# Performance work log

Hardware: AMD Instinct MI355X
Metric: run time of the kernel (lower is better)

The kernel has to match this reference:

```python
import jax, jax.numpy as jnp
import numpy as np

B, C, L = 32, 8, 2048
K, S = 512, 64  # num_shapelets, shapelets_size


def setup_inputs() -> dict:
    key = jax.random.key(0)
    k1, k2 = jax.random.split(key)
    x = jax.random.normal(k1, (B, C, L), dtype=jnp.float32)
    shapelets = jax.random.normal(k2, (C, K, S), dtype=jnp.float32)
    return {"x": x, "shapelets": shapelets}


def reference(x, shapelets):
    # x: [B, C, L]; shapelets: [C, K, S]
    s = shapelets.shape[-1]
    n_dims = x.shape[1]
    W = x.shape[2] - s + 1  # number of sliding windows
    # unfold(2, S, 1): gather overlapping windows -> [B, C, W, S]
    idx = jnp.arange(W)[:, None] + jnp.arange(s)[None, :]
    xw = x[:, :, idx]
    # L2-normalize windows along window length (clamp min like torch)
    xw = xw / jnp.maximum(jnp.linalg.norm(xw, axis=-1, keepdims=True), 1e-8)
    # L2-normalize shapelets along length
    sn = shapelets / jnp.maximum(jnp.linalg.norm(shapelets, axis=-1, keepdims=True), 1e-8)
    # matmul [B,C,W,S] @ [C,S,K] then sum over C, fused into one einsum -> [B, W, K]
    sim = jnp.einsum('bcws,cks->bwk', xw, sn) / n_dims
    sim = jax.nn.relu(sim)
    # max over window positions -> [B, K]; keep the singleton channel dim like torch ([B,1,K])
    out = jnp.max(sim, axis=1)
    return out[:, None, :]
```

## Files before the change

### kernel.cpp

```cpp
#include <hip/hip_runtime.h>


#define B_ 32
#define C_ 8
#define L_ 2048
#define K_ 512
#define S_ 64
#define W_ (L_ - S_ + 1)
#define TW 64
#define NWT ((W_ + TW - 1) / TW)
#define XP 128

typedef _Float16 f16x8 __attribute__((ext_vector_type(8)));
typedef float f32x4 __attribute__((ext_vector_type(4)));

__global__ __launch_bounds__(64)
void pack_sn_k(const float* __restrict__ sh, _Float16* __restrict__ Bp) {
    const int blk  = blockIdx.x;
    const int c    = blk >> 6;
    const int ks   = (blk >> 5) & 1;
    const int nt   = blk & 31;
    const int lane = threadIdx.x;
    const int ncol = lane & 15, quad = lane >> 4;
    const int q    = nt * 16 + ncol;

    const float4* sp = (const float4*)(sh + (size_t)(c * K_ + q) * S_);
    float ss = 0.f;
    #pragma unroll
    for (int i = 0; i < 4; ++i) {
        float4 v = sp[quad * 4 + i];
        ss += v.x * v.x + v.y * v.y + v.z * v.z + v.w * v.w;
    }
    ss += __shfl_xor(ss, 16);
    ss += __shfl_xor(ss, 32);
    float inv = 1.f / fmaxf(sqrtf(ss), 1e-8f);

    float4 u0 = sp[ks * 8 + quad * 2];
    float4 u1 = sp[ks * 8 + quad * 2 + 1];
    f16x8 o;
    o[0] = (_Float16)(u0.x * inv); o[1] = (_Float16)(u0.y * inv);
    o[2] = (_Float16)(u0.z * inv); o[3] = (_Float16)(u0.w * inv);
    o[4] = (_Float16)(u1.x * inv); o[5] = (_Float16)(u1.y * inv);
    o[6] = (_Float16)(u1.z * inv); o[7] = (_Float16)(u1.w * inv);
    ((f16x8*)Bp)[((c * 2 + ks) * 32 + nt) * 64 + lane] = o;
}

__global__ __launch_bounds__(256, 2)
void mcs_mfma_k(const float* __restrict__ x, const _Float16* __restrict__ Bp,
                float* __restrict__ out) {
    __shared__ float xl[C_ * XP];
    __shared__ float invn[C_ * TW];

    const int wt  = blockIdx.x;
    const int b   = blockIdx.y;
    const int w0  = wt * TW;
    const int tid = threadIdx.x;

    for (int i = tid; i < C_ * XP; i += 256) {
        int c = i >> 7, p = i & 127;
        int pos = w0 + p;
        float v = 0.f;
        if (p < 127 && pos < L_) v = x[(size_t)(b * C_ + c) * L_ + pos];
        xl[i] = v;
    }
    __syncthreads();

    for (int t = tid; t < C_ * TW; t += 256) {
        int c = t >> 6, m = t & 63;
        const float* p = xl + c * XP + m;
        float s0 = 0.f, s1 = 0.f, s2 = 0.f, s3 = 0.f;
        #pragma unroll
        for (int j = 0; j < S_; j += 4) {
            s0 += p[j] * p[j];     s1 += p[j + 1] * p[j + 1];
            s2 += p[j + 2] * p[j + 2]; s3 += p[j + 3] * p[j + 3];
        }
        float ss = (s0 + s1) + (s2 + s3);
        invn[t] = 0.125f / fmaxf(sqrtf(ss), 1e-8f);
    }
    __syncthreads();

    const int lane = tid & 63;
    const int wid  = tid >> 6;
    const int row  = lane & 15;
    const int quad = lane >> 4;
    const int ntb  = wid * 8;

    f32x4 acc[4][8];
    #pragma unroll
    for (int mt = 0; mt < 4; ++mt)
        #pragma unroll
        for (int nt = 0; nt < 8; ++nt)
            acc[mt][nt] = (f32x4){0.f, 0.f, 0.f, 0.f};

    #pragma unroll 1
    for (int c = 0; c < C_; ++c) {
        float iv[4];
        #pragma unroll
        for (int mt = 0; mt < 4; ++mt) iv[mt] = invn[c * TW + mt * 16 + row];

        #pragma unroll
        for (int ks = 0; ks < 2; ++ks) {
            f16x8 afr[4];
            #pragma unroll
            for (int mt = 0; mt < 4; ++mt) {
                const float* p = xl + c * XP + mt * 16 + row + ks * 32 + quad * 8;
                #pragma unroll
                for (int j = 0; j < 8; ++j)
                    afr[mt][j] = (_Float16)(p[j] * iv[mt]);
            }
            const f16x8* bpp = (const f16x8*)Bp + ((c * 2 + ks) * 32 + ntb) * 64 + lane;
            f16x8 bfr[8];
            #pragma unroll
            for (int nt = 0; nt < 8; ++nt) bfr[nt] = bpp[nt * 64];

            #pragma unroll
            for (int nt = 0; nt < 8; ++nt)
                #pragma unroll
                for (int mt = 0; mt < 4; ++mt)
                    acc[mt][nt] = __builtin_amdgcn_mfma_f32_16x16x32_f16(
                        afr[mt], bfr[nt], acc[mt][nt], 0, 0, 0);
        }
    }

    #pragma unroll
    for (int nt = 0; nt < 8; ++nt) {
        float m = 0.f;
        #pragma unroll
        for (int mt = 0; mt < 4; ++mt) {
            #pragma unroll
            for (int r = 0; r < 4; ++r) {
                int w = w0 + mt * 16 + quad * 4 + r;
                if (w < W_) m = fmaxf(m, acc[mt][nt][r]);
            }
        }
        m = fmaxf(m, __shfl_xor(m, 16));
        m = fmaxf(m, __shfl_xor(m, 32));
        if (lane < 16)
            atomicMax((unsigned int*)(out + b * K_ + (ntb + nt) * 16 + lane),
                      __float_as_uint(m));
    }
}

extern "C" void kernel_launch(void* const* d_in, const int* in_sizes, int n_in,
                              void* d_out, int out_size, void* d_ws, size_t ws_size,
                              hipStream_t stream) {
    const float* x  = (const float*)d_in[0];
    const float* sh = (const float*)d_in[1];
    float* out = (float*)d_out;
    _Float16* Bp = (_Float16*)d_ws;

    hipMemsetAsync(out, 0, (size_t)out_size * sizeof(float), stream);
    pack_sn_k<<<dim3(512), dim3(64), 0, stream>>>(sh, Bp);
    mcs_mfma_k<<<dim3(NWT, B_), dim3(256), 0, stream>>>(x, Bp, out);
}
```

Baseline: 99.89 us.

## Precompute window norms, prebuild fp16 A tiles in LDS, split K across blocks

A merged prep kernel packs normalized shapelets, computes the inverse window norms once per row with a sliding sum of squares, and zeroes the output. This replaces the memset and the separate pack launch. The main kernel splits the K dimension across a second grid axis, halving accumulators per wave so occupancy can reach 3 blocks per CU. Each channel's fp16 A fragments are built into double-buffered LDS while the MFMAs for the previous channel run. The window-validity mask is dropped, relying on zero inverse norms past W, and the sliding sum may accumulate fp32 rounding drift.

```diff
diff --git a/kernel.cpp b/kernel.cpp
--- a/kernel.cpp
+++ b/kernel.cpp
@@ -6,137 +6,166 @@
 #define L_ 2048
 #define K_ 512
 #define S_ 64
-#define W_ (L_ - S_ + 1)
+#define W_ 1985
 #define TW 64
-#define NWT ((W_ + TW - 1) / TW)
-#define XP 128
 
 typedef _Float16 f16x8 __attribute__((ext_vector_type(8)));
 typedef float f32x4 __attribute__((ext_vector_type(4)));
+typedef float f32x4u __attribute__((ext_vector_type(4), aligned(4)));
 
-__global__ __launch_bounds__(64)
-void pack_sn_k(const float* __restrict__ sh, _Float16* __restrict__ Bp) {
-    const int blk  = blockIdx.x;
-    const int c    = blk >> 6;
-    const int ks   = (blk >> 5) & 1;
-    const int nt   = blk & 31;
-    const int lane = threadIdx.x;
-    const int ncol = lane & 15, quad = lane >> 4;
-    const int q    = nt * 16 + ncol;
+__global__ __launch_bounds__(256)
+void prep_k(const float* __restrict__ x, const float* __restrict__ sh,
+            _Float16* __restrict__ Bp, float* __restrict__ invn,
+            float* __restrict__ out) {
+    __shared__ float xr[L_];
+    const int tid = threadIdx.x;
+    const int blk = blockIdx.x;
 
-    const float4* sp = (const float4*)(sh + (size_t)(c * K_ + q) * S_);
-    float ss = 0.f;
-    #pragma unroll
-    for (int i = 0; i < 4; ++i) {
-        float4 v = sp[quad * 4 + i];
-        ss += v.x * v.x + v.y * v.y + v.z * v.z + v.w * v.w;
+    if (blk < 128) {
+        const int sb   = blk * 4 + (tid >> 6);
+        const int c    = sb >> 6;
+        const int ks   = (sb >> 5) & 1;
+        const int nt   = sb & 31;
+        const int lane = tid & 63;
+        const int ncol = lane & 15, quad = lane >> 4;
+        const int q    = nt * 16 + ncol;
+
+        const float4* sp = (const float4*)(sh + (size_t)(c * K_ + q) * S_);
+        float ss = 0.f;
+        #pragma unroll
+        for (int i = 0; i < 4; ++i) {
+            float4 v = sp[quad * 4 + i];
+            ss += v.x * v.x + v.y * v.y + v.z * v.z + v.w * v.w;
+        }
+        ss += __shfl_xor(ss, 16);
+        ss += __shfl_xor(ss, 32);
+        float inv = 1.f / fmaxf(sqrtf(ss), 1e-8f);
+
+        float4 u0 = sp[ks * 8 + quad * 2];
+        float4 u1 = sp[ks * 8 + quad * 2 + 1];
+        f16x8 o;
+        o[0] = (_Float16)(u0.x * inv); o[1] = (_Float16)(u0.y * inv);
+        o[2] = (_Float16)(u0.z * inv); o[3] = (_Float16)(u0.w * inv);
+        o[4] = (_Float16)(u1.x * inv); o[5] = (_Float16)(u1.y * inv);
+        o[6] = (_Float16)(u1.z * inv); o[7] = (_Float16)(u1.w * inv);
+        ((f16x8*)Bp)[((c * 2 + ks) * 32 + nt) * 64 + lane] = o;
+    } else {
+        const int r = blk - 128;
+        const float* xp = x + (size_t)r * L_;
+        for (int i = tid; i < L_ / 4; i += 256)
+            ((float4*)xr)[i] = ((const float4*)xp)[i];
+        __syncthreads();
+
+        float* ivp = invn + (size_t)r * L_;
+        const int w0 = tid * 8;
+        float ss = 0.f;
+        if (w0 < W_) {
+            #pragma unroll
+            for (int j = 0; j < S_; ++j) { float v = xr[w0 + j]; ss += v * v; }
+        }
+        #pragma unroll
+        for (int u = 0; u < 8; ++u) {
+            int w = w0 + u;
+            float o = 0.f;
+            if (u > 0 && w < W_)
+                ss += xr[w + 63] * xr[w + 63] - xr[w - 1] * xr[w - 1];
+            if (w < W_) o = 0.125f / fmaxf(sqrtf(ss), 1e-8f);
+            if (w < L_) ivp[w] = o;
+        }
+        if (r < 64) out[r * 256 + tid] = 0.f;
     }
-    ss += __shfl_xor(ss, 16);
-    ss += __shfl_xor(ss, 32);
-    float inv = 1.f / fmaxf(sqrtf(ss), 1e-8f);
-
-    float4 u0 = sp[ks * 8 + quad * 2];
-    float4 u1 = sp[ks * 8 + quad * 2 + 1];
-    f16x8 o;
-    o[0] = (_Float16)(u0.x * inv); o[1] = (_Float16)(u0.y * inv);
-    o[2] = (_Float16)(u0.z * inv); o[3] = (_Float16)(u0.w * inv);
-    o[4] = (_Float16)(u1.x * inv); o[5] = (_Float16)(u1.y * inv);
-    o[6] = (_Float16)(u1.z * inv); o[7] = (_Float16)(u1.w * inv);
-    ((f16x8*)Bp)[((c * 2 + ks) * 32 + nt) * 64 + lane] = o;
 }
 
-__global__ __launch_bounds__(256, 2)
-void mcs_mfma_k(const float* __restrict__ x, const _Float16* __restrict__ Bp,
-                float* __restrict__ out) {
-    __shared__ float xl[C_ * XP];
-    __shared__ float invn[C_ * TW];
+__global__ __launch_bounds__(256, 3)
+void mcs_k(const float* __restrict__ x, const _Float16* __restrict__ Bp,
+           const float* __restrict__ invn, float* __restrict__ out) {
+    __shared__ float invs[C_ * TW];
+    __shared__ f16x8 Ah[2][8 * 64];
 
     const int wt  = blockIdx.x;
-    const int b   = blockIdx.y;
+    const int ng  = blockIdx.y;
+    const int b   = blockIdx.z;
     const int w0  = wt * TW;
     const int tid = threadIdx.x;
+    const int lane = tid & 63;
+    const int wv   = tid >> 6;
+    const int quad = lane >> 4;
 
-    for (int i = tid; i < C_ * XP; i += 256) {
-        int c = i >> 7, p = i & 127;
-        int pos = w0 + p;
-        float v = 0.f;
-        if (p < 127 && pos < L_) v = x[(size_t)(b * C_ + c) * L_ + pos];
-        xl[i] = v;
+    for (int i = tid; i < C_ * TW; i += 256) {
+        int c = i >> 6, w = i & 63;
+        invs[i] = invn[(size_t)(b * C_ + c) * L_ + w0 + w];
     }
+
+    auto build = [&](int cN, int bufN) {
+        const float* xrow = x + (size_t)(b * C_ + cN) * L_;
+        #pragma unroll
+        for (int it = 0; it < 2; ++it) {
+            int i   = tid + it * 256;
+            int f   = i >> 6, l = i & 63;
+            int mt  = f >> 1, ks = f & 1;
+            int row = l & 15, qd = l >> 4;
+            int m   = mt * 16 + row;
+            int p   = w0 + m + ks * 32 + qd * 8;
+            int pc  = p <= L_ - 8 ? p : L_ - 8;
+            f32x4u v0 = *(const f32x4u*)(xrow + pc);
+            f32x4u v1 = *(const f32x4u*)(xrow + pc + 4);
+            float iv = invs[cN * TW + m];
+            f16x8 o;
+            o[0] = (_Float16)(v0[0] * iv); o[1] = (_Float16)(v0[1] * iv);
+            o[2] = (_Float16)(v0[2] * iv); o[3] = (_Float16)(v0[3] * iv);
+            o[4] = (_Float16)(v1[0] * iv); o[5] = (_Float16)(v1[1] * iv);
+            o[6] = (_Float16)(v1[2] * iv); o[7] = (_Float16)(v1[3] * iv);
+            Ah[bufN][f * 64 + l] = o;
+        }
+    };
+
+    __syncthreads();
+    build(0, 0);
     __syncthreads();
 
-    for (int t = tid; t < C_ * TW; t += 256) {
-        int c = t >> 6, m = t & 63;
-        const float* p = xl + c * XP + m;
-        float s0 = 0.f, s1 = 0.f, s2 = 0.f, s3 = 0.f;
-        #pragma unroll
-        for (int j = 0; j < S_; j += 4) {
-            s0 += p[j] * p[j];     s1 += p[j + 1] * p[j + 1];
-            s2 += p[j + 2] * p[j + 2]; s3 += p[j + 3] * p[j + 3];
-        }
-        float ss = (s0 + s1) + (s2 + s3);
-        invn[t] = 0.125f / fmaxf(sqrtf(ss), 1e-8f);
-    }
-    __syncthreads();
-
-    const int lane = tid & 63;
-    const int wid  = tid >> 6;
-    const int row  = lane & 15;
-    const int quad = lane >> 4;
-    const int ntb  = wid * 8;
-
-    f32x4 acc[4][8];
+    f32x4 acc[4][4];
     #pragma unroll
     for (int mt = 0; mt < 4; ++mt)
         #pragma unroll
-        for (int nt = 0; nt < 8; ++nt)
+        for (int nt = 0; nt < 4; ++nt)
             acc[mt][nt] = (f32x4){0.f, 0.f, 0.f, 0.f};
 
-    #pragma unroll 1
+    #pragma unroll 2
     for (int c = 0; c < C_; ++c) {
-        float iv[4];
-        #pragma unroll
-        for (int mt = 0; mt < 4; ++mt) iv[mt] = invn[c * TW + mt * 16 + row];
+        const int buf = c & 1;
+        if (c + 1 < C_) build(c + 1, buf ^ 1);
 
         #pragma unroll
         for (int ks = 0; ks < 2; ++ks) {
-            f16x8 afr[4];
+            f16x8 af[4], bf[4];
+            const f16x8* bpp = (const f16x8*)Bp +
+                ((c * 2 + ks) * 32 + ng * 16 + wv * 4) * 64 + lane;
             #pragma unroll
-            for (int mt = 0; mt < 4; ++mt) {
-                const float* p = xl + c * XP + mt * 16 + row + ks * 32 + quad * 8;
-                #pragma unroll
-                for (int j = 0; j < 8; ++j)
-                    afr[mt][j] = (_Float16)(p[j] * iv[mt]);
-            }
-            const f16x8* bpp = (const f16x8*)Bp + ((c * 2 + ks) * 32 + ntb) * 64 + lane;
-            f16x8 bfr[8];
+            for (int nt = 0; nt < 4; ++nt) bf[nt] = bpp[nt * 64];
             #pragma unroll
-            for (int nt = 0; nt < 8; ++nt) bfr[nt] = bpp[nt * 64];
-
+            for (int mt = 0; mt < 4; ++mt) af[mt] = Ah[buf][(mt * 2 + ks) * 64 + lane];
             #pragma unroll
-            for (int nt = 0; nt < 8; ++nt)
+            for (int nt = 0; nt < 4; ++nt)
                 #pragma unroll
                 for (int mt = 0; mt < 4; ++mt)
                     acc[mt][nt] = __builtin_amdgcn_mfma_f32_16x16x32_f16(
-                        afr[mt], bfr[nt], acc[mt][nt], 0, 0, 0);
+                        af[mt], bf[nt], acc[mt][nt], 0, 0, 0);
         }
+        __syncthreads();
     }
 
     #pragma unroll
-    for (int nt = 0; nt < 8; ++nt) {
+    for (int nt = 0; nt < 4; ++nt) {
         float m = 0.f;
         #pragma unroll
-        for (int mt = 0; mt < 4; ++mt) {
+        for (int mt = 0; mt < 4; ++mt)
             #pragma unroll
-            for (int r = 0; r < 4; ++r) {
-                int w = w0 + mt * 16 + quad * 4 + r;
-                if (w < W_) m = fmaxf(m, acc[mt][nt][r]);
-            }
-        }
+            for (int r = 0; r < 4; ++r)
+                m = fmaxf(m, acc[mt][nt][r]);
         m = fmaxf(m, __shfl_xor(m, 16));
         m = fmaxf(m, __shfl_xor(m, 32));
         if (lane < 16)
-            atomicMax((unsigned int*)(out + b * K_ + (ntb + nt) * 16 + lane),
+            atomicMax((unsigned int*)(out + b * K_ + ng * 256 + wv * 64 + nt * 16 + lane),
                       __float_as_uint(m));
     }
 }
@@ -147,9 +176,9 @@
     const float* x  = (const float*)d_in[0];
     const float* sh = (const float*)d_in[1];
     float* out = (float*)d_out;
-    _Float16* Bp = (_Float16*)d_ws;
+    _Float16* Bp  = (_Float16*)d_ws;
+    float* invn   = (float*)((char*)d_ws + (size_t)K_ * 512 * sizeof(_Float16));
 
-    hipMemsetAsync(out, 0, (size_t)out_size * sizeof(float), stream);
-    pack_sn_k<<<dim3(512), dim3(64), 0, stream>>>(sh, Bp);
-    mcs_mfma_k<<<dim3(NWT, B_), dim3(256), 0, stream>>>(x, Bp, out);
+    prep_k<<<dim3(384), dim3(256), 0, stream>>>(x, sh, Bp, invn, out);
+    mcs_k<<<dim3(32, 2, B_), dim3(256), 0, stream>>>(x, Bp, invn, out);
 }
```

Result: slower. 106.1 us (+6.3%).
